# Optimization experiments

Hardware: AMD Instinct MI355X
Metric: run time of the kernel (lower is better)

The kernel has to match this reference:

```python
import jax, jax.numpy as jnp
import numpy as np
from jax import lax


def setup_inputs() -> dict:
    key = jax.random.key(0)
    k1, k2, k3, k4, k5 = jax.random.split(key, 5)
    B, Cin, Cout, H, W, K, S = 16, 256, 256, 128, 128, 3, 512
    x = jax.random.normal(k1, (B, Cin, H, W), dtype=jnp.float32)
    style = jax.random.normal(k2, (B, S), dtype=jnp.float32)
    # parameters (kaiming-ish scales)
    conv_w = jax.random.normal(k3, (Cout, Cin, K, K), dtype=jnp.float32) * (1.0 / np.sqrt(Cin * K * K))
    fc_w = jax.random.normal(k4, (Cout, S), dtype=jnp.float32) * (1.0 / np.sqrt(S))
    fc_b = jax.random.normal(k5, (Cout,), dtype=jnp.float32) * 0.01
    return {"x": x, "style": style, "conv_w": conv_w, "fc_w": fc_w, "fc_b": fc_b}


def reference(x, style, conv_w, fc_w, fc_b):
    # style_fc: (B, S) @ (S, Cout) + b -> per-sample per-output-channel scale
    s = style @ fc_w.T + fc_b  # (B, Cout)
    # Modulating W[o] by s[b,o] on the output-channel axis commutes with the
    # convolution, so the per-sample loop is a single conv + channel scale.
    # (Original uses F.conv2d with bias=None, so conv bias is never applied.)
    y = lax.conv_general_dilated(
        x, conv_w,
        window_strides=(1, 1),
        padding=[(1, 1), (1, 1)],
        dimension_numbers=("NCHW", "OIHW", "NCHW"),
    )  # (B, Cout, H, W)
    return y * s[:, :, None, None]
```

## Files before the change

kernel.cpp:

```cpp
#include <hip/hip_runtime.h>
#include <stdint.h>

typedef __attribute__((ext_vector_type(8))) short bf16x8;
typedef __attribute__((ext_vector_type(8))) unsigned short u16x8;
typedef __attribute__((ext_vector_type(4))) float f32x4;
typedef __attribute__((ext_vector_type(2))) float f32x2;

#define NB   16
#define CIN  256
#define COUT 256
#define HH   128
#define WW   128
#define SDIM 512

#define BM 256
#define BN 128
#define BK 64
#define KPAD 72
#define NCOL 130

#define A_BYTES (BM * KPAD * 2)
#define B_BYTES (3 * NCOL * KPAD * 2)
#define S_BYTES (COUT * 4)
#define LDS_BYTES (A_BYTES + B_BYTES + S_BYTES)

__device__ __forceinline__ unsigned short f2bf(float f) {
    unsigned int u = __float_as_uint(f);
    u += 0x7fff + ((u >> 16) & 1);
    return (unsigned short)(u >> 16);
}

__global__ void style_fc_kernel(const float* __restrict__ style,
                                const float* __restrict__ fc_w,
                                const float* __restrict__ fc_b,
                                float* __restrict__ s_out) {
    const int b = blockIdx.x;
    const int co = threadIdx.x;
    const f32x4* st = (const f32x4*)(style + b * SDIM);
    const f32x4* w  = (const f32x4*)(fc_w + co * SDIM);
    float acc = fc_b[co];
    #pragma unroll 4
    for (int k = 0; k < SDIM / 4; ++k) {
        f32x4 a = st[k], c = w[k];
        acc += a.x * c.x + a.y * c.y + a.z * c.z + a.w * c.w;
    }
    s_out[b * COUT + co] = acc;
}

__global__ void wt_transform_kernel(const float* __restrict__ conv_w,
                                    unsigned short* __restrict__ wt) {
    const int tid = blockIdx.x * blockDim.x + threadIdx.x;
    const int co = tid >> 8;
    const int ci = tid & 255;
    const float* src = conv_w + (co * CIN + ci) * 9;
    const int q = ci >> 6;
    const int kl = ci & 63;
    #pragma unroll
    for (int t = 0; t < 9; ++t) {
        wt[(((t * 4 + q) * COUT + co) << 6) + kl] = f2bf(src[t]);
    }
}

__global__ void __launch_bounds__(512, 2)
modconv_kernel(const float* __restrict__ x,
               const unsigned short* __restrict__ wt,
               const float* __restrict__ s,
               float* __restrict__ out) {
    extern __shared__ char lds[];
    unsigned short* Al = (unsigned short*)lds;
    unsigned short* Bl = (unsigned short*)(lds + A_BYTES);
    float* Sl = (float*)(lds + A_BYTES + B_BYTES);

    const int tid  = threadIdx.x;
    const int lane = tid & 63;
    const int wid  = tid >> 6;
    const int bb   = blockIdx.x >> 7;
    const int h    = blockIdx.x & 127;

    {
        f32x4 z = {0.f, 0.f, 0.f, 0.f};
        for (int i = tid; i < B_BYTES / 16; i += 512)
            *(f32x4*)(lds + A_BYTES + i * 16) = z;
    }
    if (tid < COUT) Sl[tid] = s[bb * COUT + tid];
    __syncthreads();

    f32x4 acc[4][4];
    {
        f32x4 z = {0.f, 0.f, 0.f, 0.f};
        #pragma unroll
        for (int mi = 0; mi < 4; ++mi)
            #pragma unroll
            for (int nj = 0; nj < 4; ++nj)
                acc[mi][nj] = z;
    }

    const int wm = wid >> 1;
    const int wn = wid & 1;
    const int cobase = wm * 64;
    const int wbase  = wn * 64;
    const int l15 = lane & 15;
    const int kl8 = (lane >> 4) * 8;

    const int p = tid & 63;
    const int g = wid;

    #pragma unroll 1
    for (int q = 0; q < 4; ++q) {
        #pragma unroll
        for (int kh = 0; kh < 3; ++kh) {
            const int r = h + kh - 1;
            if (r >= 0 && r < HH) {
                const float* xr = x + (((size_t)(bb * CIN + q * 64 + g * 8) * HH + r) * WW) + p * 2;
                u16x8 v0, v1;
                #pragma unroll
                for (int j = 0; j < 8; ++j) {
                    f32x2 v = *(const f32x2*)(xr + j * (HH * WW));
                    v0[j] = f2bf(v.x);
                    v1[j] = f2bf(v.y);
                }
                unsigned short* d = Bl + (kh * NCOL + 1 + p * 2) * KPAD + g * 8;
                *(u16x8*)d = v0;
                *(u16x8*)(d + KPAD) = v1;
            }
        }
        #pragma unroll 1
        for (int t = 0; t < 9; ++t) {
            const unsigned short* wsrc = wt + (t * 4 + q) * (BM * 64);
            #pragma unroll
            for (int it = 0; it < 4; ++it) {
                const int c = it * 512 + tid;
                const int co = c >> 3;
                const int sub = c & 7;
                u16x8 v = *(const u16x8*)(wsrc + c * 8);
                *(u16x8*)(Al + co * KPAD + sub * 8) = v;
            }
            __syncthreads();

            const int kh = t / 3;
            const int kw = t - kh * 3;
            #pragma unroll
            for (int kk = 0; kk < BK; kk += 32) {
                bf16x8 a[4], b[4];
                #pragma unroll
                for (int mi = 0; mi < 4; ++mi)
                    a[mi] = *(const bf16x8*)(Al + (cobase + mi * 16 + l15) * KPAD + kk + kl8);
                #pragma unroll
                for (int nj = 0; nj < 4; ++nj)
                    b[nj] = *(const bf16x8*)(Bl + (kh * NCOL + wbase + nj * 16 + l15 + kw) * KPAD + kk + kl8);
                #pragma unroll
                for (int mi = 0; mi < 4; ++mi)
                    #pragma unroll
                    for (int nj = 0; nj < 4; ++nj)
                        acc[mi][nj] = __builtin_amdgcn_mfma_f32_16x16x32_bf16(
                            a[mi], b[nj], acc[mi][nj], 0, 0, 0);
            }
            __syncthreads();
        }
    }

    const int rowD = (lane >> 4) * 4;
    #pragma unroll
    for (int mi = 0; mi < 4; ++mi) {
        #pragma unroll
        for (int r = 0; r < 4; ++r) {
            const int co = cobase + mi * 16 + rowD + r;
            const float sv = Sl[co];
            float* orow = out + (((size_t)(bb * COUT + co) * HH + h) * WW);
            #pragma unroll
            for (int nj = 0; nj < 4; ++nj)
                orow[wbase + nj * 16 + l15] = acc[mi][nj][r] * sv;
        }
    }
}

extern "C" void kernel_launch(void* const* d_in, const int* in_sizes, int n_in,
                              void* d_out, int out_size, void* d_ws, size_t ws_size,
                              hipStream_t stream) {
    const float* x      = (const float*)d_in[0];
    const float* style  = (const float*)d_in[1];
    const float* conv_w = (const float*)d_in[2];
    const float* fc_w   = (const float*)d_in[3];
    const float* fc_b   = (const float*)d_in[4];
    float* out = (float*)d_out;

    float* s_ws = (float*)d_ws;
    unsigned short* wt = (unsigned short*)((char*)d_ws + 16384);

    hipFuncSetAttribute(reinterpret_cast<const void*>(modconv_kernel),
                        hipFuncAttributeMaxDynamicSharedMemorySize, LDS_BYTES);

    style_fc_kernel<<<NB, COUT, 0, stream>>>(style, fc_w, fc_b, s_ws);
    wt_transform_kernel<<<(COUT * CIN) / 256, 256, 0, stream>>>(conv_w, wt);
    modconv_kernel<<<NB * HH, 512, LDS_BYTES, stream>>>(x, wt, s_ws, out);
}
```

Measured before the change: 1.003 ms.

## Load conv weights directly from global into registers, drop LDS weight staging

Removes the per-tap LDS staging of the weight tile: each wave now reads its A fragments straight from the global (L2-cached) transformed weight buffer, which drops the two barriers per tap and shrinks LDS use. Occupancy is raised to 4 blocks per CU, blocks are swizzled across batch/rows, the input-row load is restructured for coalesced per-lane reads, and the weight transform kernel is rewritten to stage through shared memory for coalesced writes. The risk is higher global/L2 traffic and latency on weight reads that are no longer shared through LDS, and register pressure from the tighter launch bound.

```diff
diff --git a/kernel.cpp b/kernel.cpp
--- a/kernel.cpp
+++ b/kernel.cpp
@@ -4,7 +4,6 @@
 typedef __attribute__((ext_vector_type(8))) short bf16x8;
 typedef __attribute__((ext_vector_type(8))) unsigned short u16x8;
 typedef __attribute__((ext_vector_type(4))) float f32x4;
-typedef __attribute__((ext_vector_type(2))) float f32x2;
 
 #define NB   16
 #define CIN  256
@@ -13,16 +12,13 @@
 #define WW   128
 #define SDIM 512
 
-#define BM 256
-#define BN 128
 #define BK 64
 #define KPAD 72
 #define NCOL 130
 
-#define A_BYTES (BM * KPAD * 2)
 #define B_BYTES (3 * NCOL * KPAD * 2)
 #define S_BYTES (COUT * 4)
-#define LDS_BYTES (A_BYTES + B_BYTES + S_BYTES)
+#define LDS_BYTES (B_BYTES + S_BYTES)
 
 __device__ __forceinline__ unsigned short f2bf(float f) {
     unsigned int u = __float_as_uint(f);
@@ -49,41 +45,48 @@
 
 __global__ void wt_transform_kernel(const float* __restrict__ conv_w,
                                     unsigned short* __restrict__ wt) {
-    const int tid = blockIdx.x * blockDim.x + threadIdx.x;
-    const int co = tid >> 8;
-    const int ci = tid & 255;
-    const float* src = conv_w + (co * CIN + ci) * 9;
-    const int q = ci >> 6;
-    const int kl = ci & 63;
+    __shared__ unsigned short T[9][256];
+    const int co = blockIdx.x;
+    const int ci = threadIdx.x;
+    const float* src = conv_w + ((size_t)co * CIN + ci) * 9;
+    float v[9];
     #pragma unroll
-    for (int t = 0; t < 9; ++t) {
-        wt[(((t * 4 + q) * COUT + co) << 6) + kl] = f2bf(src[t]);
+    for (int t = 0; t < 9; ++t) v[t] = src[t];
+    #pragma unroll
+    for (int t = 0; t < 9; ++t) T[t][ci] = f2bf(v[t]);
+    __syncthreads();
+    const unsigned int* T32 = (const unsigned int*)&T[0][0];
+    unsigned int* out32 = (unsigned int*)wt;
+    for (int idx = ci; idx < 1152; idx += 256) {
+        const int d = idx & 31;
+        const int r = idx >> 5;
+        out32[(((size_t)r * COUT + co) << 5) + d] = T32[idx];
     }
 }
 
-__global__ void __launch_bounds__(512, 2)
+__global__ void __launch_bounds__(512, 4)
 modconv_kernel(const float* __restrict__ x,
                const unsigned short* __restrict__ wt,
                const float* __restrict__ s,
                float* __restrict__ out) {
     extern __shared__ char lds[];
-    unsigned short* Al = (unsigned short*)lds;
-    unsigned short* Bl = (unsigned short*)(lds + A_BYTES);
-    float* Sl = (float*)(lds + A_BYTES + B_BYTES);
+    unsigned short* Bl = (unsigned short*)lds;
+    float* Sl = (float*)(lds + B_BYTES);
 
     const int tid  = threadIdx.x;
     const int lane = tid & 63;
     const int wid  = tid >> 6;
-    const int bb   = blockIdx.x >> 7;
-    const int h    = blockIdx.x & 127;
+    const int bid  = blockIdx.x;
+    const int nid  = (bid & 7) * 256 + (bid >> 3);
+    const int bb   = nid >> 7;
+    const int h    = nid & 127;
 
     {
         f32x4 z = {0.f, 0.f, 0.f, 0.f};
         for (int i = tid; i < B_BYTES / 16; i += 512)
-            *(f32x4*)(lds + A_BYTES + i * 16) = z;
+            *(f32x4*)(lds + i * 16) = z;
     }
     if (tid < COUT) Sl[tid] = s[bb * COUT + tid];
-    __syncthreads();
 
     f32x4 acc[4][4];
     {
@@ -102,49 +105,40 @@
     const int l15 = lane & 15;
     const int kl8 = (lane >> 4) * 8;
 
-    const int p = tid & 63;
-    const int g = wid;
+    __syncthreads();
 
     #pragma unroll 1
     for (int q = 0; q < 4; ++q) {
+        if (q) __syncthreads();
         #pragma unroll
         for (int kh = 0; kh < 3; ++kh) {
             const int r = h + kh - 1;
             if (r >= 0 && r < HH) {
-                const float* xr = x + (((size_t)(bb * CIN + q * 64 + g * 8) * HH + r) * WW) + p * 2;
-                u16x8 v0, v1;
+                const float* xs = x + (((size_t)(bb * CIN + q * 64 + wid * 8)) * HH + r) * WW;
                 #pragma unroll
-                for (int j = 0; j < 8; ++j) {
-                    f32x2 v = *(const f32x2*)(xr + j * (HH * WW));
-                    v0[j] = f2bf(v.x);
-                    v1[j] = f2bf(v.y);
+                for (int half = 0; half < 2; ++half) {
+                    const int w = lane + half * 64;
+                    u16x8 vv;
+                    #pragma unroll
+                    for (int j = 0; j < 8; ++j)
+                        vv[j] = f2bf(xs[j * (HH * WW) + w]);
+                    *(u16x8*)(Bl + (kh * NCOL + 1 + w) * KPAD + wid * 8) = vv;
                 }
-                unsigned short* d = Bl + (kh * NCOL + 1 + p * 2) * KPAD + g * 8;
-                *(u16x8*)d = v0;
-                *(u16x8*)(d + KPAD) = v1;
             }
         }
-        #pragma unroll 1
+        __syncthreads();
+        #pragma unroll 3
         for (int t = 0; t < 9; ++t) {
-            const unsigned short* wsrc = wt + (t * 4 + q) * (BM * 64);
-            #pragma unroll
-            for (int it = 0; it < 4; ++it) {
-                const int c = it * 512 + tid;
-                const int co = c >> 3;
-                const int sub = c & 7;
-                u16x8 v = *(const u16x8*)(wsrc + c * 8);
-                *(u16x8*)(Al + co * KPAD + sub * 8) = v;
-            }
-            __syncthreads();
-
             const int kh = t / 3;
             const int kw = t - kh * 3;
+            const unsigned short* wsrc = wt + ((size_t)(t * 4 + q) * COUT + cobase) * 64;
             #pragma unroll
-            for (int kk = 0; kk < BK; kk += 32) {
+            for (int kkid = 0; kkid < 2; ++kkid) {
+                const int kk = kkid * 32;
                 bf16x8 a[4], b[4];
                 #pragma unroll
                 for (int mi = 0; mi < 4; ++mi)
-                    a[mi] = *(const bf16x8*)(Al + (cobase + mi * 16 + l15) * KPAD + kk + kl8);
+                    a[mi] = *(const bf16x8*)(wsrc + (mi * 16 + l15) * 64 + kk + kl8);
                 #pragma unroll
                 for (int nj = 0; nj < 4; ++nj)
                     b[nj] = *(const bf16x8*)(Bl + (kh * NCOL + wbase + nj * 16 + l15 + kw) * KPAD + kk + kl8);
@@ -155,7 +149,6 @@
                         acc[mi][nj] = __builtin_amdgcn_mfma_f32_16x16x32_bf16(
                             a[mi], b[nj], acc[mi][nj], 0, 0, 0);
             }
-            __syncthreads();
         }
     }
 
@@ -187,10 +180,7 @@
     float* s_ws = (float*)d_ws;
     unsigned short* wt = (unsigned short*)((char*)d_ws + 16384);
 
-    hipFuncSetAttribute(reinterpret_cast<const void*>(modconv_kernel),
-                        hipFuncAttributeMaxDynamicSharedMemorySize, LDS_BYTES);
-
     style_fc_kernel<<<NB, COUT, 0, stream>>>(style, fc_w, fc_b, s_ws);
-    wt_transform_kernel<<<(COUT * CIN) / 256, 256, 0, stream>>>(conv_w, wt);
+    wt_transform_kernel<<<COUT, 256, 0, stream>>>(conv_w, wt);
     modconv_kernel<<<NB * HH, 512, LDS_BYTES, stream>>>(x, wt, s_ws, out);
 }
```

New measurement: 950.9 us. -5.2%, faster.
